# Kernel optimization log

Measured on AMD Instinct MI355X. Metric: run time of the kernel, lower is better.

## Reference

```python
import jax, jax.numpy as jnp
import numpy as np

HEADS = 16
HEAD_SIZE = 64
INF = 1e12  # bert4keras K.infinity() uses a large finite value


def _rotate_interleaved(x):
    # result[..., 2i] = -x[..., 2i+1]; result[..., 2i+1] = x[..., 2i]
    x2 = jnp.stack([-x[..., 1::2], x[..., ::2]], axis=-1)
    return x2.reshape(x.shape)


def setup_inputs() -> dict:
    key = jax.random.key(0)
    k1, k2 = jax.random.split(key)
    B, N, D = 8, 1024, 1024
    x = jax.random.normal(k1, (B, N, D), dtype=jnp.float32)
    W = jax.random.normal(k2, (D, 2 * HEADS * HEAD_SIZE), dtype=jnp.float32) * (1.0 / np.sqrt(D))
    b = jnp.zeros((2 * HEADS * HEAD_SIZE,), dtype=jnp.float32)
    seq_mask = jnp.ones((B, N), dtype=jnp.float32)
    return {"x": x, "W": W, "b": b, "seq_mask": seq_mask}


def reference(x, W, b, seq_mask):
    B, N, _ = x.shape
    H, d = HEADS, HEAD_SIZE
    proj = x @ W + b                       # [B, N, 2*H*d]
    z = proj.reshape(B, N, H, 2 * d)       # split into heads then stack
    qw, kw = z[..., :d], z[..., d:]        # [B, N, H, d]

    # RoPE (interleaved sin/cos)
    pos = jnp.arange(N, dtype=jnp.float32)
    freqs = jnp.power(10000.0, -2.0 * jnp.arange(d // 2, dtype=jnp.float32) / d)
    ang = pos[:, None] * freqs[None, :]    # [N, d/2]
    cos_pos = jnp.repeat(jnp.cos(ang), 2, axis=-1)[None, :, None, :]  # [1,N,1,d]
    sin_pos = jnp.repeat(jnp.sin(ang), 2, axis=-1)[None, :, None, :]
    qw = qw * cos_pos + _rotate_interleaved(qw) * sin_pos
    kw = kw * cos_pos + _rotate_interleaved(kw) * sin_pos

    logits = jnp.einsum('bmhd,bnhd->bhmn', qw, kw)   # [B, H, N, N]

    # sequence masking on query (axis 2) and key (axis 3)
    logits = logits - (1.0 - seq_mask[:, None, :, None]) * INF
    logits = logits - (1.0 - seq_mask[:, None, None, :]) * INF

    # triangular mask: keep upper triangle including diagonal
    tri = jnp.triu(jnp.ones((N, N), dtype=logits.dtype))
    logits = logits - (1.0 - tri) * INF
    return logits / jnp.sqrt(jnp.float32(d))
```

## Files before the change

kernel.cpp:

```cpp
#include <hip/hip_runtime.h>

typedef __bf16 bf16;
typedef __bf16 bf16x4 __attribute__((ext_vector_type(4)));
typedef __bf16 bf16x8 __attribute__((ext_vector_type(8)));
typedef float f32x4 __attribute__((ext_vector_type(4)));

#define GL(p) ((const __attribute__((address_space(1))) void*)(p))
#define LD(p) ((__attribute__((address_space(3))) void*)(p))

__global__ __launch_bounds__(256) void k_prep(
    const float4* __restrict__ x4, bf16x4* __restrict__ o4,
    const float* __restrict__ W, bf16* __restrict__ Wt,
    float* __restrict__ cost, float* __restrict__ sint)
{
    __shared__ bf16 tile[64][65];
    const int bid = (int)blockIdx.x;
    const int t = threadIdx.x;
    if (bid < 2048) {
        for (int i = bid * 256 + t; i < 2097152; i += 2048 * 256) {
            float4 v = x4[i];
            bf16x4 o;
            o[0] = (bf16)v.x; o[1] = (bf16)v.y; o[2] = (bf16)v.z; o[3] = (bf16)v.w;
            o4[i] = o;
        }
    } else if (bid < 2560) {
        const int wid = bid - 2048;
        const int k0 = (wid & 15) * 64;
        const int n0 = (wid >> 4) * 64;
        const int c = t & 63, r4 = t >> 6;
#pragma unroll
        for (int p = 0; p < 16; ++p) {
            int r = p * 4 + r4;
            tile[r][c] = (bf16)W[(size_t)(k0 + r) * 2048 + n0 + c];
        }
        __syncthreads();
#pragma unroll
        for (int p = 0; p < 16; ++p) {
            int n = p * 4 + r4;
            Wt[(size_t)(n0 + n) * 1024 + k0 + c] = tile[c][n];
        }
    } else {
        int idx = (bid - 2560) * 256 + t;
        int pos = idx >> 5, i = idx & 31;
        float freq = powf(10000.f, -(float)i / 32.f);
        float ang = (float)pos * freq;
        cost[idx] = cosf(ang);
        sint[idx] = sinf(ang);
    }
}

__global__ __launch_bounds__(512) void k_gemm1(
    const bf16* __restrict__ Xb, const bf16* __restrict__ Wt,
    const float* __restrict__ bias,
    const float* __restrict__ cost, const float* __restrict__ sint,
    bf16* __restrict__ Qb, bf16* __restrict__ Kb)
{
    __shared__ bf16 lA[2][256 * 64];
    __shared__ bf16 lB[2][128 * 64];
    const int t = threadIdx.x;
    const int lane = t & 63;
    const int wave = t >> 6;
    const int wr = (wave >> 1) * 64;
    const int wc = (wave & 1) * 64;
    const int bm = (int)blockIdx.x * 256;
    const int bn = (int)blockIdx.y * 128;
    const int rl = lane & 15;
    const int hi = lane >> 4;

    f32x4 acc[4][4] = {};

#define STAGE1(kt, c) do {                                                              \
    _Pragma("unroll")                                                                   \
    for (int p = 0; p < 4; ++p) {                                                       \
        int e = t * 8 + p * 4096;                                                       \
        int row = e >> 6; int g = (e >> 3) & 7;                                         \
        __builtin_amdgcn_global_load_lds(                                               \
            GL(Xb + (size_t)(bm + row) * 1024 + (kt) * 64 + ((g ^ (row & 7)) << 3)),    \
            LD(&lA[c][e]), 16, 0, 0);                                                   \
    }                                                                                   \
    _Pragma("unroll")                                                                   \
    for (int p = 0; p < 2; ++p) {                                                       \
        int e = t * 8 + p * 4096;                                                       \
        int row = e >> 6; int g = (e >> 3) & 7;                                         \
        __builtin_amdgcn_global_load_lds(                                               \
            GL(Wt + (size_t)(bn + row) * 1024 + (kt) * 64 + ((g ^ (row & 7)) << 3)),    \
            LD(&lB[c][e]), 16, 0, 0);                                                   \
    }                                                                                   \
} while (0)

    STAGE1(0, 0);
    STAGE1(1, 1);
    asm volatile("s_waitcnt vmcnt(6)" ::: "memory");
    __builtin_amdgcn_sched_barrier(0);
    __builtin_amdgcn_s_barrier();
    asm volatile("" ::: "memory");

    for (int kt = 0; kt < 16; ++kt) {
        const int cur = kt & 1;
        bf16x8 af[2][4], bfr[2][4];
#pragma unroll
        for (int ks = 0; ks < 2; ++ks) {
#pragma unroll
            for (int m = 0; m < 4; ++m) {
                int R = wr + m * 16 + rl;
                af[ks][m] = *(const bf16x8*)&lA[cur][(R << 6) + (((ks * 4 + hi) ^ (R & 7)) << 3)];
            }
#pragma unroll
            for (int n = 0; n < 4; ++n) {
                int S = wc + n * 16 + rl;
                bfr[ks][n] = *(const bf16x8*)&lB[cur][(S << 6) + (((ks * 4 + hi) ^ (S & 7)) << 3)];
            }
        }
#pragma unroll
        for (int ks = 0; ks < 2; ++ks)
#pragma unroll
            for (int m = 0; m < 4; ++m)
#pragma unroll
                for (int n = 0; n < 4; ++n)
                    acc[m][n] = __builtin_amdgcn_mfma_f32_16x16x32_bf16(af[ks][m], bfr[ks][n], acc[m][n], 0, 0, 0);

        if (kt < 15) {
            __builtin_amdgcn_s_barrier();
            if (kt + 2 < 16) {
                STAGE1(kt + 2, cur);
                asm volatile("s_waitcnt vmcnt(6)" ::: "memory");
            } else {
                asm volatile("s_waitcnt vmcnt(0)" ::: "memory");
            }
            __builtin_amdgcn_sched_barrier(0);
            __builtin_amdgcn_s_barrier();
            asm volatile("" ::: "memory");
        }
    }
#undef STAGE1

#pragma unroll
    for (int m = 0; m < 4; ++m) {
#pragma unroll
        for (int n = 0; n < 4; ++n) {
            int colg = bn + wc + n * 16 + rl;
            float bv = bias[colg];
            int h = colg >> 7;
            int rem = colg & 127;
            int qk = rem >> 6;
            int dcol = rem & 63;
            int fi = dcol >> 1;
            float sgn = (dcol & 1) ? 1.f : -1.f;
            bf16* dstb = qk ? Kb : Qb;
#pragma unroll
            for (int r = 0; r < 4; ++r) {
                int rowg = bm + wr + m * 16 + hi * 4 + r;
                int pos = rowg & 1023, bidx = rowg >> 10;
                float val = acc[m][n][r] + bv;
                float part = __shfl_xor(val, 1);
                float cv = cost[pos * 32 + fi], sv = sint[pos * 32 + fi];
                float outv = val * cv + sgn * part * sv;
                dstb[(((size_t)(bidx * 16 + h)) * 1024 + pos) * 64 + dcol] = (bf16)outv;
            }
        }
    }
}

__global__ __launch_bounds__(256) void k_gemm2(
    const bf16* __restrict__ Qb, const bf16* __restrict__ Kb,
    const float* __restrict__ smask, float* __restrict__ out)
{
    __shared__ bf16 lQ[128 * 64];
    __shared__ bf16 lK[128 * 64];
    const int t = threadIdx.x;
    const int lane = t & 63, wave = t >> 6;
    const int wr = (wave >> 1) * 64, wc = (wave & 1) * 64;
    const int bid = (int)blockIdx.x;
    const int bh = bid >> 6;
    const int tile = bid & 63;
    const int bm = (tile >> 3) * 128;
    const int bn = (tile & 7) * 128;
    const int b = bh >> 4;
    const int rl = lane & 15, rq = lane >> 4;
    const float NINF = 1.25e11f;

    if (bn + 128 <= bm) {
#pragma unroll
        for (int m = 0; m < 4; ++m) {
#pragma unroll
            for (int r = 0; r < 4; ++r) {
                int mg = bm + wr + m * 16 + rq * 4 + r;
                float mpen = 1.f - smask[b * 1024 + mg];
                size_t rowoff = ((size_t)bh * 1024 + mg) * 1024;
#pragma unroll
                for (int n = 0; n < 4; ++n) {
                    int ng = bn + wc + n * 16 + rl;
                    float npen = 1.f - smask[b * 1024 + ng];
                    out[rowoff + ng] = -(mpen + npen + 1.f) * NINF;
                }
            }
        }
        return;
    }

    const size_t qoff = (size_t)bh * 1024 * 64;
#pragma unroll
    for (int p = 0; p < 4; ++p) {
        int e = t * 8 + p * 2048;
        __builtin_amdgcn_global_load_lds(GL(Qb + qoff + (size_t)bm * 64 + e), LD(&lQ[e]), 16, 0, 0);
        __builtin_amdgcn_global_load_lds(GL(Kb + qoff + (size_t)bn * 64 + e), LD(&lK[e]), 16, 0, 0);
    }
    __syncthreads();

    f32x4 acc[4][4] = {};
    const int kg = rq * 8;
#pragma unroll
    for (int ks = 0; ks < 2; ++ks) {
        bf16x8 af[4], bfr[4];
#pragma unroll
        for (int m = 0; m < 4; ++m) af[m] = *(const bf16x8*)&lQ[(wr + m * 16 + rl) * 64 + ks * 32 + kg];
#pragma unroll
        for (int n = 0; n < 4; ++n) bfr[n] = *(const bf16x8*)&lK[(wc + n * 16 + rl) * 64 + ks * 32 + kg];
#pragma unroll
        for (int m = 0; m < 4; ++m)
#pragma unroll
            for (int n = 0; n < 4; ++n)
                acc[m][n] = __builtin_amdgcn_mfma_f32_16x16x32_bf16(af[m], bfr[n], acc[m][n], 0, 0, 0);
    }

#pragma unroll
    for (int m = 0; m < 4; ++m) {
#pragma unroll
        for (int r = 0; r < 4; ++r) {
            int mg = bm + wr + m * 16 + rq * 4 + r;
            float mpen = 1.f - smask[b * 1024 + mg];
            size_t rowoff = ((size_t)bh * 1024 + mg) * 1024;
#pragma unroll
            for (int n = 0; n < 4; ++n) {
                int ng = bn + wc + n * 16 + rl;
                float npen = 1.f - smask[b * 1024 + ng];
                float pen = mpen + npen + ((ng < mg) ? 1.f : 0.f);
                out[rowoff + ng] = acc[m][n][r] * 0.125f - pen * NINF;
            }
        }
    }
}

extern "C" void kernel_launch(void* const* d_in, const int* in_sizes, int n_in,
                              void* d_out, int out_size, void* d_ws, size_t ws_size,
                              hipStream_t stream) {
    (void)in_sizes; (void)n_in; (void)out_size; (void)ws_size;
    const float* x    = (const float*)d_in[0];
    const float* W    = (const float*)d_in[1];
    const float* bias = (const float*)d_in[2];
    const float* sm   = (const float*)d_in[3];
    float* out = (float*)d_out;

    char* ws = (char*)d_ws;
    size_t o = 0;
    bf16* Xb = (bf16*)(ws + o); o += 8388608ull * 2;
    bf16* Wt = (bf16*)(ws + o); o += 2097152ull * 2;
    bf16* Qb = (bf16*)(ws + o); o += 8388608ull * 2;
    bf16* Kb = (bf16*)(ws + o); o += 8388608ull * 2;
    float* cost = (float*)(ws + o); o += 32768ull * 4;
    float* sint = (float*)(ws + o); o += 32768ull * 4;

    hipLaunchKernelGGL(k_prep, dim3(2688), dim3(256), 0, stream,
                       (const float4*)x, (bf16x4*)Xb, W, Wt, cost, sint);
    hipLaunchKernelGGL(k_gemm1, dim3(32, 16), dim3(512), 0, stream,
                       Xb, Wt, bias, cost, sint, Qb, Kb);
    hipLaunchKernelGGL(k_gemm2, dim3(8192), dim3(256), 0, stream,
                       Qb, Kb, sm, out);
}
```

Baseline: 193.9 us.

## Split projection GEMM k-loop into barrier-synced LDS-read/MFMA phases with priority

Splits each k-tile of the projection GEMM into four phases: a few LDS fragment reads, then a barrier, then eight MFMAs at raised wave priority, then a barrier. The aim is to interleave LDS traffic and matrix work across waves in a ping-pong style and to cut register pressure from holding all 16 fragments at once. The trade-off is eight extra workgroup barriers per k-tile, which can serialize waves if they do not line up well.

Measured after the change: 205.0 us. 1.06x slower.

```diff
diff --git a/kernel.cpp b/kernel.cpp
--- a/kernel.cpp
+++ b/kernel.cpp
@@ -88,6 +88,33 @@
     }                                                                                   \
 } while (0)
 
+#define RD_A(ks, m) (*(const bf16x8*)&lA[cur][((wr + (m) * 16 + rl) << 6) + \
+    ((((ks) * 4 + hi) ^ ((wr + (m) * 16 + rl) & 7)) << 3)])
+#define RD_B(ks, n) (*(const bf16x8*)&lB[cur][((wc + (n) * 16 + rl) << 6) + \
+    ((((ks) * 4 + hi) ^ ((wc + (n) * 16 + rl) & 7)) << 3)])
+
+#define PHASE_SYNC() do {                                      \
+    __builtin_amdgcn_s_barrier();                              \
+    asm volatile("s_waitcnt lgkmcnt(0)" ::: "memory");         \
+    __builtin_amdgcn_sched_barrier(0);                         \
+    __builtin_amdgcn_s_setprio(1);                             \
+} while (0)
+
+#define PHASE_END() do {                                       \
+    __builtin_amdgcn_s_setprio(0);                             \
+    __builtin_amdgcn_s_barrier();                              \
+} while (0)
+
+#define MFMA8(ks, n0_)                                                                           \
+    acc[0][n0_]     = __builtin_amdgcn_mfma_f32_16x16x32_bf16(a0, b0, acc[0][n0_], 0, 0, 0);     \
+    acc[1][n0_]     = __builtin_amdgcn_mfma_f32_16x16x32_bf16(a1, b0, acc[1][n0_], 0, 0, 0);     \
+    acc[2][n0_]     = __builtin_amdgcn_mfma_f32_16x16x32_bf16(a2, b0, acc[2][n0_], 0, 0, 0);     \
+    acc[3][n0_]     = __builtin_amdgcn_mfma_f32_16x16x32_bf16(a3, b0, acc[3][n0_], 0, 0, 0);     \
+    acc[0][n0_ + 1] = __builtin_amdgcn_mfma_f32_16x16x32_bf16(a0, b1, acc[0][n0_ + 1], 0, 0, 0); \
+    acc[1][n0_ + 1] = __builtin_amdgcn_mfma_f32_16x16x32_bf16(a1, b1, acc[1][n0_ + 1], 0, 0, 0); \
+    acc[2][n0_ + 1] = __builtin_amdgcn_mfma_f32_16x16x32_bf16(a2, b1, acc[2][n0_ + 1], 0, 0, 0); \
+    acc[3][n0_ + 1] = __builtin_amdgcn_mfma_f32_16x16x32_bf16(a3, b1, acc[3][n0_ + 1], 0, 0, 0)
+
     STAGE1(0, 0);
     STAGE1(1, 1);
     asm volatile("s_waitcnt vmcnt(6)" ::: "memory");
@@ -97,30 +124,27 @@
 
     for (int kt = 0; kt < 16; ++kt) {
         const int cur = kt & 1;
-        bf16x8 af[2][4], bfr[2][4];
-#pragma unroll
-        for (int ks = 0; ks < 2; ++ks) {
-#pragma unroll
-            for (int m = 0; m < 4; ++m) {
-                int R = wr + m * 16 + rl;
-                af[ks][m] = *(const bf16x8*)&lA[cur][(R << 6) + (((ks * 4 + hi) ^ (R & 7)) << 3)];
-            }
-#pragma unroll
-            for (int n = 0; n < 4; ++n) {
-                int S = wc + n * 16 + rl;
-                bfr[ks][n] = *(const bf16x8*)&lB[cur][(S << 6) + (((ks * 4 + hi) ^ (S & 7)) << 3)];
-            }
-        }
-#pragma unroll
-        for (int ks = 0; ks < 2; ++ks)
-#pragma unroll
-            for (int m = 0; m < 4; ++m)
-#pragma unroll
-                for (int n = 0; n < 4; ++n)
-                    acc[m][n] = __builtin_amdgcn_mfma_f32_16x16x32_bf16(af[ks][m], bfr[ks][n], acc[m][n], 0, 0, 0);
+        bf16x8 a0, a1, a2, a3, b0, b1;
+        a0 = RD_A(0, 0); a1 = RD_A(0, 1); a2 = RD_A(0, 2); a3 = RD_A(0, 3);
+        b0 = RD_B(0, 0); b1 = RD_B(0, 1);
+        PHASE_SYNC();
+        MFMA8(0, 0);
+        PHASE_END();
+        b0 = RD_B(0, 2); b1 = RD_B(0, 3);
+        PHASE_SYNC();
+        MFMA8(0, 2);
+        PHASE_END();
+        a0 = RD_A(1, 0); a1 = RD_A(1, 1); a2 = RD_A(1, 2); a3 = RD_A(1, 3);
+        b0 = RD_B(1, 0); b1 = RD_B(1, 1);
+        PHASE_SYNC();
+        MFMA8(1, 0);
+        PHASE_END();
+        b0 = RD_B(1, 2); b1 = RD_B(1, 3);
+        PHASE_SYNC();
+        MFMA8(1, 2);
+        PHASE_END();
 
         if (kt < 15) {
-            __builtin_amdgcn_s_barrier();
             if (kt + 2 < 16) {
                 STAGE1(kt + 2, cur);
                 asm volatile("s_waitcnt vmcnt(6)" ::: "memory");
@@ -133,6 +157,11 @@
         }
     }
 #undef STAGE1
+#undef RD_A
+#undef RD_B
+#undef PHASE_SYNC
+#undef PHASE_END
+#undef MFMA8
 
 #pragma unroll
     for (int m = 0; m < 4; ++m) {
```
